# Performance work log

Hardware: AMD Instinct MI355X
Metric: run time of the kernel (lower is better)

Reference implementation:

```python
import jax, jax.numpy as jnp
import numpy as np

M = 16       # learned queries
K = 64       # top-k sparse tokens
HEADS = 4    # attention heads
LN_EPS = 1e-5


def _l2norm(x, eps=1e-12):
    n = jnp.linalg.norm(x, axis=-1, keepdims=True)
    return x / jnp.maximum(n, eps)


def _layernorm(x, w, b):
    mu = x.mean(-1, keepdims=True)
    var = x.var(-1, keepdims=True)
    return (x - mu) * jax.lax.rsqrt(var + LN_EPS) * w + b


def setup_inputs() -> dict:
    key = jax.random.key(0)
    ks = jax.random.split(key, 12)
    B, N, C, T, TD, D = 4, 16384, 1024, 20, 512, 64
    s = lambda k, sh: jax.random.normal(k, sh, jnp.float32) * 0.02
    return {
        "image_features": jax.random.normal(ks[0], (B, N, C), jnp.float32),
        "text_features": jax.random.normal(ks[1], (B, T, TD), jnp.float32),
        "Wd": s(ks[2], (C, D)), "bd": jnp.zeros((D,), jnp.float32),
        "Wu": s(ks[3], (D, C)), "bu": jnp.zeros((C,), jnp.float32),
        "m_queries": jax.random.normal(ks[4], (1, M, D), jnp.float32),
        "Wq": s(ks[5], (D, D)), "bq": jnp.zeros((D,), jnp.float32),
        "Wk": s(ks[6], (D, D)), "bk": jnp.zeros((D,), jnp.float32),
        "Wv": s(ks[7], (D, D)), "bv": jnp.zeros((D,), jnp.float32),
        "Wo": s(ks[8], (D, D)), "bo": jnp.zeros((D,), jnp.float32),
        "ln_w": jnp.ones((D,), jnp.float32), "ln_b": jnp.zeros((D,), jnp.float32),
        "gamma": jnp.float32(0.1),
    }


def reference(image_features, text_features, Wd, bd, Wu, bu, m_queries,
              Wq, bq, Wk, bk, Wv, bv, Wo, bo, ln_w, ln_b, gamma):
    B, N, C = image_features.shape
    D = Wd.shape[1]
    identity = image_features

    # down-project + exact GELU (dropout is identity at eval)
    a = jax.nn.gelu(image_features @ Wd + bd, approximate=False)  # [B,N,D]

    # tokens_of_interest=None, text_consistency_loss=False:
    # slice text to projected dim, take token 0 as key
    sel = text_features[:, 0, :D]                                  # [B,D]
    scores = jnp.einsum("bnd,bd->bn", _l2norm(a), _l2norm(sel))    # [B,N]

    # top-k mask -> nonzero gives row-sorted indices per batch
    _, idx = jax.lax.top_k(scores, K)                              # [B,K]
    idx = jnp.sort(idx, axis=1)

    sparse = jnp.take_along_axis(a, idx[:, :, None], axis=1)       # [B,K,D]
    queries = jnp.broadcast_to(m_queries, (B, M, D))
    comb = jnp.concatenate([queries, sparse], axis=1)              # [B,M+K,D]

    x = _layernorm(comb, ln_w, ln_b)
    H, Dh = HEADS, D // HEADS
    S = M + K
    q = (x @ Wq + bq).reshape(B, S, H, Dh)
    k = (x @ Wk + bk).reshape(B, S, H, Dh)
    v = (x @ Wv + bv).reshape(B, S, H, Dh)
    att = jnp.einsum("bshd,bthd->bhst", q, k) / jnp.sqrt(jnp.float32(Dh))
    att = jax.nn.softmax(att, axis=-1)
    o = jnp.einsum("bhst,bthd->bshd", att, v).reshape(B, S, D)
    attn_out = o @ Wo + bo

    enh = comb + attn_out
    enh_sparse = enh[:, M:, :]                                     # [B,K,D]

    # scatter enhanced sparse tokens back into full sequence
    brow = jnp.arange(B)[:, None]
    delta_proj = jnp.zeros_like(a).at[brow, idx].set(enh_sparse)   # [B,N,D]
    delta_x = delta_proj @ Wu + bu                                 # [B,N,C]

    return identity + delta_x * gamma
```

## Files before the change

kernel.cpp:

```cpp
#include <hip/hip_runtime.h>
#include <hip/hip_bf16.h>
#include <math.h>

typedef __bf16 bf16x8 __attribute__((ext_vector_type(8)));
typedef unsigned short u16x8 __attribute__((ext_vector_type(8)));
typedef float f32x4 __attribute__((ext_vector_type(4)));

#define CDIM 1024
#define DDIM 64
#define NB   16384
#define NROWS 65536

__device__ __forceinline__ unsigned short f2bf(float x){
  unsigned int u = __float_as_uint(x);
  unsigned int lsb = (u >> 16) & 1u;
  u += 0x7fffu + lsb;
  return (unsigned short)(u >> 16);
}

__device__ __forceinline__ void load_lds16(const float* g, float* l){
  __builtin_amdgcn_global_load_lds(
      (const __attribute__((address_space(1))) void*)g,
      (__attribute__((address_space(3))) void*)l, 16, 0, 0);
}

__global__ __launch_bounds__(256) void dsa_prep(
    const float* __restrict__ Wd, const float* __restrict__ tf,
    const float* __restrict__ bu, const float* __restrict__ gam,
    unsigned short* __restrict__ Wf, float* __restrict__ seln,
    float* __restrict__ gbu){
  int bb = blockIdx.x, tid = threadIdx.x;
  if (bb < 32){
    int g = bb*256 + tid;
    int lane = g & 63, tj = g >> 6;
    int n  = ((tj & 3) << 4) + (lane & 15);
    int k0 = ((tj >> 2) << 5) + ((lane >> 4) << 3);
    u16x8 uv;
    #pragma unroll
    for (int e=0;e<8;e++) uv[e] = f2bf(Wd[(k0+e)*DDIM + n]);
    *(u16x8*)(Wf + (size_t)g*8) = uv;
  } else {
    int w = tid >> 6, lane = tid & 63;
    float x = tf[w*(20*512) + lane];
    float sq = x*x;
    #pragma unroll
    for (int m=1; m<64; m<<=1) sq += __shfl_xor(sq, m);
    seln[w*64 + lane] = x / fmaxf(sqrtf(sq), 1e-12f);
    float g = gam[0];
    f32x4 b4 = *(const f32x4*)(bu + tid*4);
    *(f32x4*)(gbu + tid*4) = g*b4;
  }
}

__global__ __launch_bounds__(256, 4) void dsa_main(
    const float* __restrict__ X, const unsigned short* __restrict__ Wf,
    const float* __restrict__ bd, const float* __restrict__ gbu,
    const float* __restrict__ seln,
    float* __restrict__ out, float* __restrict__ a_out, float* __restrict__ scores)
{
  __shared__ __align__(16) float AsF[8192];
  __shared__ __align__(16) float gbS[1024];
  const int tid  = threadIdx.x;
  const int lane = tid & 63, w = tid >> 6;
  const int lr = lane & 15, lq = lane >> 4;
  const int row0 = blockIdx.x*64 + w*16;
  const int batch = blockIdx.x >> 8;

  { f32x4 t = *(const f32x4*)(gbu + tid*4); *(f32x4*)(gbS + tid*4) = t; }
  __syncthreads();

  const int rsub = lane >> 4;
  const int ch   = lane & 15;
  const float* gbase = X + (size_t)(row0 + rsub)*CDIM;
  float* asw = AsF + w*2048;
  float* op  = out + (size_t)(row0 + lr)*CDIM;
  const bf16x8* wf8 = (const bf16x8*)Wf;

  bf16x8 B[8];
  f32x4 acc[4] = {};

#define DMA(P, SL) { \
    { int gc = ch ^ ((0*4 + rsub)&7); \
      load_lds16(gbase + (size_t)(0*4)*CDIM + (P)*64 + gc*4, asw + (SL)*1024 + 0*256); } \
    { int gc = ch ^ ((1*4 + rsub)&7); \
      load_lds16(gbase + (size_t)(1*4)*CDIM + (P)*64 + gc*4, asw + (SL)*1024 + 1*256); } \
    { int gc = ch ^ ((2*4 + rsub)&7); \
      load_lds16(gbase + (size_t)(2*4)*CDIM + (P)*64 + gc*4, asw + (SL)*1024 + 2*256); } \
    { int gc = ch ^ ((3*4 + rsub)&7); \
      load_lds16(gbase + (size_t)(3*4)*CDIM + (P)*64 + gc*4, asw + (SL)*1024 + 3*256); } }

#define LDB(P) { \
    B[0] = wf8[(((P)*2+0)*4+0)*64 + lane]; \
    B[1] = wf8[(((P)*2+0)*4+1)*64 + lane]; \
    B[2] = wf8[(((P)*2+0)*4+2)*64 + lane]; \
    B[3] = wf8[(((P)*2+0)*4+3)*64 + lane]; \
    B[4] = wf8[(((P)*2+1)*4+0)*64 + lane]; \
    B[5] = wf8[(((P)*2+1)*4+1)*64 + lane]; \
    B[6] = wf8[(((P)*2+1)*4+2)*64 + lane]; \
    B[7] = wf8[(((P)*2+1)*4+3)*64 + lane]; }

#define STEP(P, S, SL) { \
    int c0 = (((S)*8 + lq*2 + 0) ^ (lr & 7)); \
    int c1 = (((S)*8 + lq*2 + 1) ^ (lr & 7)); \
    f32x4 xa = *(const f32x4*)(asw + (SL)*1024 + lr*64 + c0*4); \
    f32x4 xb = *(const f32x4*)(asw + (SL)*1024 + lr*64 + c1*4); \
    f32x4 g0 = *(const f32x4*)(gbS + (P)*64 + (S)*32 + lq*8); \
    f32x4 g1 = *(const f32x4*)(gbS + (P)*64 + (S)*32 + lq*8 + 4); \
    *(f32x4*)(op + (P)*64 + (S)*32 + lq*8)     = xa + g0; \
    *(f32x4*)(op + (P)*64 + (S)*32 + lq*8 + 4) = xb + g1; \
    bf16x8 av; \
    av[0]=(__bf16)xa[0]; av[1]=(__bf16)xa[1]; av[2]=(__bf16)xa[2]; av[3]=(__bf16)xa[3]; \
    av[4]=(__bf16)xb[0]; av[5]=(__bf16)xb[1]; av[6]=(__bf16)xb[2]; av[7]=(__bf16)xb[3]; \
    acc[0] = __builtin_amdgcn_mfma_f32_16x16x32_bf16(av, B[4*(S)+0], acc[0], 0,0,0); \
    acc[1] = __builtin_amdgcn_mfma_f32_16x16x32_bf16(av, B[4*(S)+1], acc[1], 0,0,0); \
    acc[2] = __builtin_amdgcn_mfma_f32_16x16x32_bf16(av, B[4*(S)+2], acc[2], 0,0,0); \
    acc[3] = __builtin_amdgcn_mfma_f32_16x16x32_bf16(av, B[4*(S)+3], acc[3], 0,0,0); }

#define PH(P) { \
    DMA((P)+1, ((P)+1)&1) \
    LDB(P) \
    asm volatile("s_waitcnt vmcnt(12)" ::: "memory"); \
    STEP(P, 0, (P)&1) STEP(P, 1, (P)&1) \
    asm volatile("" ::: "memory"); }

  DMA(0, 0)
  PH(0)  PH(1)  PH(2)  PH(3)  PH(4)  PH(5)  PH(6)  PH(7)
  PH(8)  PH(9)  PH(10) PH(11) PH(12) PH(13) PH(14)
  LDB(15)
  asm volatile("s_waitcnt vmcnt(8)" ::: "memory");
  STEP(15, 0, 1) STEP(15, 1, 1)

#undef DMA
#undef LDB
#undef STEP
#undef PH

  const float* selb = seln + batch*64;
  float ss[4] = {0,0,0,0}, dt[4] = {0,0,0,0};
  float gv[4][4];
  #pragma unroll
  for (int j=0;j<4;j++){
    int col = 16*j + lr;
    float bdc = bd[col];
    float sc  = selb[col];
    #pragma unroll
    for (int r=0;r<4;r++){
      float y = acc[j][r] + bdc;
      float g = 0.5f * y * (1.0f + erff(y * 0.70710678118654752f));
      gv[j][r] = g;
      ss[r] += g*g;
      dt[r] += g*sc;
    }
  }
  #pragma unroll
  for (int r=0;r<4;r++){
    int row = row0 + 4*lq + r;
    #pragma unroll
    for (int j=0;j<4;j++)
      a_out[(size_t)row*DDIM + 16*j + lr] = gv[j][r];
  }
  #pragma unroll
  for (int m=1;m<16;m<<=1){
    #pragma unroll
    for (int r=0;r<4;r++){
      ss[r] += __shfl_xor(ss[r], m);
      dt[r] += __shfl_xor(dt[r], m);
    }
  }
  if (lr == 0){
    #pragma unroll
    for (int r=0;r<4;r++)
      scores[row0 + 4*lq + r] = dt[r] / fmaxf(sqrtf(ss[r]), 1e-12f);
  }
}

__global__ __launch_bounds__(1024) void dsa_topk(const float* __restrict__ scores,
                                                 int* __restrict__ idxo){
  const int b = blockIdx.x, tid = threadIdx.x;
  const float* s = scores + b*NB;
  const int base = tid*16;
  unsigned key[16];
  #pragma unroll
  for (int i=0;i<16;i+=4){
    f32x4 f = *(const f32x4*)(s + base + i);
    #pragma unroll
    for (int c=0;c<4;c++){
      unsigned u = __float_as_uint(f[c]);
      key[i+c] = (u & 0x80000000u) ? ~u : (u | 0x80000000u);
    }
  }

  __shared__ unsigned bins[256];
  __shared__ unsigned sh_pref, sh_R;
  __shared__ int selIdx[64];
  __shared__ int eqIdx[256];
  __shared__ unsigned selCnt, eqCnt;

  unsigned prefix = 0, R = 64;
  for (int pass=0; pass<4; ++pass){
    const int shift = 24 - pass*8;
    if (tid < 256) bins[tid] = 0;
    __syncthreads();
    #pragma unroll
    for (int i=0;i<16;i++){
      unsigned k = key[i];
      bool ok;
      if (pass == 0) ok = true;
      else           ok = ((k >> (shift+8)) == prefix);
      if (ok) atomicAdd(&bins[(k >> shift) & 255u], 1u);
    }
    __syncthreads();
    if (tid < 64){
      unsigned c0 = bins[tid*4+0], c1 = bins[tid*4+1];
      unsigned c2 = bins[tid*4+2], c3 = bins[tid*4+3];
      unsigned gs = c0+c1+c2+c3;
      unsigned suf = gs;
      #pragma unroll
      for (int m=1;m<64;m<<=1){
        unsigned o = __shfl_down(suf, m);
        if (tid + m < 64) suf += o;
      }
      unsigned above = suf - gs;
      if (above < R && R <= suf){
        unsigned a3 = above;
        unsigned a2 = a3 + c3;
        unsigned a1 = a2 + c2;
        unsigned a0 = a1 + c1;
        unsigned bb, ab;
        if      (R <= a3 + c3){ bb = 3; ab = a3; }
        else if (R <= a2 + c2){ bb = 2; ab = a2; }
        else if (R <= a1 + c1){ bb = 1; ab = a1; }
        else                  { bb = 0; ab = a0; }
        sh_pref = (prefix << 8) | (tid*4 + bb);
        sh_R = R - ab;
      }
    }
    __syncthreads();
    prefix = sh_pref; R = sh_R;
    __syncthreads();
  }
  if (tid == 0){ selCnt = 0; eqCnt = 0; }
  __syncthreads();
  #pragma unroll
  for (int i=0;i<16;i++){
    unsigned k = key[i];
    if (k > prefix){
      selIdx[atomicAdd(&selCnt, 1u)] = base + i;
    } else if (k == prefix){
      unsigned p = atomicAdd(&eqCnt, 1u);
      if (p < 256) eqIdx[p] = base + i;
    }
  }
  __syncthreads();
  if (tid == 0){
    unsigned n = eqCnt < 256u ? eqCnt : 256u;
    unsigned have = selCnt;
    for (unsigned r2 = 0; r2 < R; ++r2){
      int best = 0x7fffffff, bi = -1;
      for (unsigned e=0; e<n; e++)
        if (eqIdx[e] < best){ best = eqIdx[e]; bi = (int)e; }
      selIdx[have + r2] = best;
      eqIdx[bi] = 0x7fffffff;
    }
  }
  __syncthreads();
  if (tid < 64){
    int x = selIdx[tid];
    #pragma unroll
    for (int size=2; size<=64; size<<=1){
      #pragma unroll
      for (int stride=size>>1; stride>0; stride>>=1){
        int ox = __shfl_xor(x, stride);
        bool up = ((tid & size) == 0);
        bool takeMin = (((tid & stride) == 0) == up);
        int mn = x < ox ? x : ox, mx = x < ox ? ox : x;
        x = takeMin ? mn : mx;
      }
    }
    idxo[b*64 + tid] = x;
  }
}

__global__ __launch_bounds__(512) void dsa_tail(
    const float* __restrict__ a, const float* __restrict__ mq, const int* __restrict__ idx,
    const float* __restrict__ lnw, const float* __restrict__ lnb,
    const float* __restrict__ Wq, const float* __restrict__ bq,
    const float* __restrict__ Wk, const float* __restrict__ bk,
    const float* __restrict__ Wv, const float* __restrict__ bv,
    const float* __restrict__ Wo, const float* __restrict__ bo,
    float* __restrict__ enh)
{
  __shared__ float xln[80][64];
  __shared__ float qS[80][64];
  __shared__ float vS[80][68];
  __shared__ float kT[64][81];
  __shared__ float oS[80][64];
  __shared__ float WoS[64][64];
  __shared__ float rowbuf[8][84];
  __shared__ int   sidx[64];

  const int b = blockIdx.x, tid = threadIdx.x;
  const int w = tid >> 6, lane = tid & 63;

  if (tid < 64) sidx[tid] = idx[b*64 + tid];
  for (int e = tid; e < 4096; e += 512) WoS[e>>6][e&63] = Wo[e];
  __syncthreads();

  {
    float lw = lnw[lane], lb = lnb[lane];
    float vals[10];
    #pragma unroll
    for (int i=0;i<10;i++){
      int s = w + 8*i;
      vals[i] = (s < 16) ? mq[s*64 + lane]
                         : a[((size_t)b*NB + sidx[s-16])*64 + lane];
    }
    #pragma unroll
    for (int i=0;i<10;i++){
      int s = w + 8*i;
      float val = vals[i];
      float sm = val, sq = val*val;
      #pragma unroll
      for (int m=1;m<64;m<<=1){ sm += __shfl_xor(sm,m); sq += __shfl_xor(sq,m); }
      float mu  = sm * (1.0f/64.0f);
      float var = sq * (1.0f/64.0f) - mu*mu;
      xln[s][lane] = (val - mu) * rsqrtf(var + 1e-5f) * lw + lb;
    }
  }
  __syncthreads();

  #pragma unroll 1
  for (int m = 0; m < 3; ++m){
    const float* Wm = (m==0) ? Wq : (m==1) ? Wk : Wv;
    const float* bm = (m==0) ? bq : (m==1) ? bk : bv;
    float wreg[64];
    #pragma unroll
    for (int c=0;c<64;c++) wreg[c] = Wm[c*64 + lane];
    float bias = bm[lane];
    #pragma unroll 1
    for (int s = w; s < 80; s += 8){
      float accv = bias;
      #pragma unroll
      for (int c4=0;c4<16;c4++){
        f32x4 x4 = *(const f32x4*)&xln[s][c4*4];
        accv += x4[0]*wreg[c4*4+0] + x4[1]*wreg[c4*4+1]
              + x4[2]*wreg[c4*4+2] + x4[3]*wreg[c4*4+3];
      }
      if (m==0)      qS[s][lane]  = accv;
      else if (m==1) kT[lane][s]  = accv;
      else           vS[s][lane]  = accv;
    }
  }
  __syncthreads();

  {
    const int h = w >> 1, h16 = h*16;
    const int i0 = 16 + (w & 1)*32;
    const int jj = lane >> 4, dd = lane & 15;
    #pragma unroll 2
    for (int ii = 0; ii < 32; ++ii){
      int i = i0 + ii;
      float v0 = 0.f, v1 = 0.f;
      #pragma unroll
      for (int d=0; d<16; ++d){
        float qd = qS[i][h16+d];
        v0 = fmaf(qd, kT[h16+d][lane],    v0);
        v1 = fmaf(qd, kT[h16+d][64 + dd], v1);
      }
      v0 *= 0.25f; v1 *= 0.25f;
      float mx = fmaxf(v0, v1);
      #pragma unroll
      for (int m2=1;m2<64;m2<<=1) mx = fmaxf(mx, __shfl_xor(mx,m2));
      float e0 = expf(v0 - mx);
      float e1 = expf(v1 - mx);
      float sm = e0 + ((lane < 16) ? e1 : 0.f);
      #pragma unroll
      for (int m2=1;m2<64;m2<<=1) sm += __shfl_xor(sm,m2);
      float inv = 1.0f / sm;
      rowbuf[w][lane] = e0 * inv;
      if (lane < 16) rowbuf[w][64+dd] = e1 * inv;
      float part = 0.f;
      #pragma unroll
      for (int tt=0; tt<20; ++tt){
        int j = jj*20 + tt;
        part = fmaf(rowbuf[w][j], vS[j][h16+dd], part);
      }
      part += __shfl_xor(part, 16);
      part += __shfl_xor(part, 32);
      if (lane < 16) oS[i][h16+dd] = part;
    }
  }
  __syncthreads();

  for (int e = tid; e < 4096; e += 512){
    int s16 = e >> 6, cc = e & 63;
    float accv = bo[cc];
    #pragma unroll
    for (int d4=0; d4<16; ++d4){
      f32x4 o4 = *(const f32x4*)&oS[16+s16][d4*4];
      accv += o4[0]*WoS[d4*4+0][cc] + o4[1]*WoS[d4*4+1][cc]
            + o4[2]*WoS[d4*4+2][cc] + o4[3]*WoS[d4*4+3][cc];
    }
    float cmb = a[((size_t)b*NB + sidx[s16])*64 + cc];
    enh[(b*64 + s16)*64 + cc] = cmb + accv;
  }
}

__global__ __launch_bounds__(256) void dsa_scatter(
    const float* __restrict__ enh, const float* __restrict__ Wu,
    const float* __restrict__ gam, const int* __restrict__ idx,
    float* __restrict__ out)
{
  int blk = blockIdx.x;
  int b = blk >> 6, j = blk & 63;
  int tid = threadIdx.x;
  __shared__ float er[64];
  if (tid < 64) er[tid] = enh[(b*64+j)*64 + tid];
  __syncthreads();
  int n = idx[b*64 + j];
  float gamma = gam[0];
  int c0 = tid*4;
  float ax=0.f, ay=0.f, az=0.f, aw=0.f;
  #pragma unroll 8
  for (int d=0; d<64; ++d){
    float ev = er[d];
    f32x4 wr = *(const f32x4*)(Wu + d*CDIM + c0);
    ax += ev*wr[0]; ay += ev*wr[1]; az += ev*wr[2]; aw += ev*wr[3];
  }
  float* op = out + ((size_t)b*NB + n)*CDIM + c0;
  f32x4 cu = *(f32x4*)op;
  cu[0] += gamma*ax; cu[1] += gamma*ay; cu[2] += gamma*az; cu[3] += gamma*aw;
  *(f32x4*)op = cu;
}

extern "C" void kernel_launch(void* const* d_in, const int* in_sizes, int n_in,
                              void* d_out, int out_size, void* d_ws, size_t ws_size,
                              hipStream_t stream) {
  const float* X    = (const float*)d_in[0];
  const float* tf   = (const float*)d_in[1];
  const float* Wd   = (const float*)d_in[2];
  const float* bd   = (const float*)d_in[3];
  const float* Wu   = (const float*)d_in[4];
  const float* bu   = (const float*)d_in[5];
  const float* mq   = (const float*)d_in[6];
  const float* Wq   = (const float*)d_in[7];
  const float* bq   = (const float*)d_in[8];
  const float* Wk   = (const float*)d_in[9];
  const float* bk   = (const float*)d_in[10];
  const float* Wv   = (const float*)d_in[11];
  const float* bv   = (const float*)d_in[12];
  const float* Wo   = (const float*)d_in[13];
  const float* bo   = (const float*)d_in[14];
  const float* lnw  = (const float*)d_in[15];
  const float* lnb  = (const float*)d_in[16];
  const float* gam  = (const float*)d_in[17];
  float* out = (float*)d_out;

  float* ws_a               = (float*)d_ws;
  unsigned short* ws_wf     = (unsigned short*)(ws_a + (size_t)NROWS*DDIM);
  float* ws_scores          = (float*)(ws_wf + 64*CDIM);
  float* ws_seln            = ws_scores + NROWS;
  float* ws_gbu             = ws_seln + 256;
  int*   ws_idx             = (int*)(ws_gbu + 1024);
  float* ws_enh             = (float*)(ws_idx + 256);

  dsa_prep   <<<33,   256, 0, stream>>>(Wd, tf, bu, gam, ws_wf, ws_seln, ws_gbu);
  dsa_main   <<<1024, 256, 0, stream>>>(X, ws_wf, bd, ws_gbu, ws_seln,
                                        out, ws_a, ws_scores);
  dsa_topk   <<<4,   1024, 0, stream>>>(ws_scores, ws_idx);
  dsa_tail   <<<4,    512, 0, stream>>>(ws_a, mq, ws_idx, lnw, lnb,
                                        Wq, bq, Wk, bk, Wv, bv, Wo, bo, ws_enh);
  dsa_scatter<<<256,  256, 0, stream>>>(ws_enh, Wu, gam, ws_idx, out);
}
```

Measured before the change: 220.8 us.

## Split identity+bias copy out of GEMM kernel and re-pipeline the Wd loads

The residual write (out = X + gamma*bu) moves out of the fused GEMM/score kernel into a separate streaming copy kernel, so X is now read from HBM twice. The GEMM kernel's software pipeline is also reordered: B fragments for the next phase are prefetched after compute and the vmcnt waits are adjusted. The intent is to make the GEMM loop leaner and let the copy run as a simple bandwidth-bound pass, at the cost of an extra full read of the 256MB input.

```diff
diff --git a/kernel.cpp b/kernel.cpp
--- a/kernel.cpp
+++ b/kernel.cpp
@@ -52,28 +52,22 @@
   }
 }
 
-__global__ __launch_bounds__(256, 4) void dsa_main(
+__global__ __launch_bounds__(256, 4) void dsa_gemm(
     const float* __restrict__ X, const unsigned short* __restrict__ Wf,
-    const float* __restrict__ bd, const float* __restrict__ gbu,
-    const float* __restrict__ seln,
-    float* __restrict__ out, float* __restrict__ a_out, float* __restrict__ scores)
+    const float* __restrict__ bd, const float* __restrict__ seln,
+    float* __restrict__ a_out, float* __restrict__ scores)
 {
   __shared__ __align__(16) float AsF[8192];
-  __shared__ __align__(16) float gbS[1024];
   const int tid  = threadIdx.x;
   const int lane = tid & 63, w = tid >> 6;
   const int lr = lane & 15, lq = lane >> 4;
   const int row0 = blockIdx.x*64 + w*16;
   const int batch = blockIdx.x >> 8;
 
-  { f32x4 t = *(const f32x4*)(gbu + tid*4); *(f32x4*)(gbS + tid*4) = t; }
-  __syncthreads();
-
   const int rsub = lane >> 4;
   const int ch   = lane & 15;
   const float* gbase = X + (size_t)(row0 + rsub)*CDIM;
   float* asw = AsF + w*2048;
-  float* op  = out + (size_t)(row0 + lr)*CDIM;
   const bf16x8* wf8 = (const bf16x8*)Wf;
 
   bf16x8 B[8];
@@ -87,7 +81,8 @@
     { int gc = ch ^ ((2*4 + rsub)&7); \
       load_lds16(gbase + (size_t)(2*4)*CDIM + (P)*64 + gc*4, asw + (SL)*1024 + 2*256); } \
     { int gc = ch ^ ((3*4 + rsub)&7); \
-      load_lds16(gbase + (size_t)(3*4)*CDIM + (P)*64 + gc*4, asw + (SL)*1024 + 3*256); } }
+      load_lds16(gbase + (size_t)(3*4)*CDIM + (P)*64 + gc*4, asw + (SL)*1024 + 3*256); } \
+    asm volatile("" ::: "memory"); }
 
 #define LDB(P) { \
     B[0] = wf8[(((P)*2+0)*4+0)*64 + lane]; \
@@ -99,15 +94,11 @@
     B[6] = wf8[(((P)*2+1)*4+2)*64 + lane]; \
     B[7] = wf8[(((P)*2+1)*4+3)*64 + lane]; }
 
-#define STEP(P, S, SL) { \
+#define STEP(S, SL) { \
     int c0 = (((S)*8 + lq*2 + 0) ^ (lr & 7)); \
     int c1 = (((S)*8 + lq*2 + 1) ^ (lr & 7)); \
     f32x4 xa = *(const f32x4*)(asw + (SL)*1024 + lr*64 + c0*4); \
     f32x4 xb = *(const f32x4*)(asw + (SL)*1024 + lr*64 + c1*4); \
-    f32x4 g0 = *(const f32x4*)(gbS + (P)*64 + (S)*32 + lq*8); \
-    f32x4 g1 = *(const f32x4*)(gbS + (P)*64 + (S)*32 + lq*8 + 4); \
-    *(f32x4*)(op + (P)*64 + (S)*32 + lq*8)     = xa + g0; \
-    *(f32x4*)(op + (P)*64 + (S)*32 + lq*8 + 4) = xb + g1; \
     bf16x8 av; \
     av[0]=(__bf16)xa[0]; av[1]=(__bf16)xa[1]; av[2]=(__bf16)xa[2]; av[3]=(__bf16)xa[3]; \
     av[4]=(__bf16)xb[0]; av[5]=(__bf16)xb[1]; av[6]=(__bf16)xb[2]; av[7]=(__bf16)xb[3]; \
@@ -116,19 +107,24 @@
     acc[2] = __builtin_amdgcn_mfma_f32_16x16x32_bf16(av, B[4*(S)+2], acc[2], 0,0,0); \
     acc[3] = __builtin_amdgcn_mfma_f32_16x16x32_bf16(av, B[4*(S)+3], acc[3], 0,0,0); }
 
-#define PH(P) { \
+#define PH(P, W1) { \
+    asm volatile("s_waitcnt vmcnt(" W1 ")" ::: "memory"); \
     DMA((P)+1, ((P)+1)&1) \
-    LDB(P) \
-    asm volatile("s_waitcnt vmcnt(12)" ::: "memory"); \
-    STEP(P, 0, (P)&1) STEP(P, 1, (P)&1) \
+    asm volatile("s_waitcnt vmcnt(4)" ::: "memory"); \
+    STEP(0, (P)&1) STEP(1, (P)&1) \
+    LDB((P)+1) \
     asm volatile("" ::: "memory"); }
 
   DMA(0, 0)
-  PH(0)  PH(1)  PH(2)  PH(3)  PH(4)  PH(5)  PH(6)  PH(7)
-  PH(8)  PH(9)  PH(10) PH(11) PH(12) PH(13) PH(14)
-  LDB(15)
+  LDB(0)
+  DMA(1, 1)
+  PH(0,"12")
+  PH(1,"8")  PH(2,"8")  PH(3,"8")  PH(4,"8")  PH(5,"8")
+  PH(6,"8")  PH(7,"8")  PH(8,"8")  PH(9,"8")  PH(10,"8")
+  PH(11,"8") PH(12,"8") PH(13,"8") PH(14,"8")
   asm volatile("s_waitcnt vmcnt(8)" ::: "memory");
-  STEP(15, 0, 1) STEP(15, 1, 1)
+  asm volatile("s_waitcnt vmcnt(0)" ::: "memory");
+  STEP(0, 1) STEP(1, 1)
 
 #undef DMA
 #undef LDB
@@ -172,6 +168,20 @@
     for (int r=0;r<4;r++)
       scores[row0 + 4*lq + r] = dt[r] / fmaxf(sqrtf(ss[r]), 1e-12f);
   }
+}
+
+__global__ __launch_bounds__(256) void dsa_copy(
+    const float* __restrict__ X, const float* __restrict__ gbu,
+    float* __restrict__ out)
+{
+  const f32x4* x4 = (const f32x4*)X;
+  f32x4*       o4 = (f32x4*)out;
+  const f32x4  gb = ((const f32x4*)gbu)[threadIdx.x];
+  size_t i = (size_t)blockIdx.x*256 + threadIdx.x;
+  const size_t S = (size_t)2048*256;
+  #pragma unroll 8
+  for (int k = 0; k < 32; ++k, i += S)
+    o4[i] = x4[i] + gb;
 }
 
 __global__ __launch_bounds__(1024) void dsa_topk(const float* __restrict__ scores,
@@ -465,10 +475,10 @@
   float* ws_enh             = (float*)(ws_idx + 256);
 
   dsa_prep   <<<33,   256, 0, stream>>>(Wd, tf, bu, gam, ws_wf, ws_seln, ws_gbu);
-  dsa_main   <<<1024, 256, 0, stream>>>(X, ws_wf, bd, ws_gbu, ws_seln,
-                                        out, ws_a, ws_scores);
+  dsa_gemm   <<<1024, 256, 0, stream>>>(X, ws_wf, bd, ws_seln, ws_a, ws_scores);
   dsa_topk   <<<4,   1024, 0, stream>>>(ws_scores, ws_idx);
   dsa_tail   <<<4,    512, 0, stream>>>(ws_a, mq, ws_idx, lnw, lnb,
                                         Wq, bq, Wk, bk, Wv, bv, Wo, bo, ws_enh);
+  dsa_copy   <<<2048, 256, 0, stream>>>(X, ws_gbu, out);
   dsa_scatter<<<256,  256, 0, stream>>>(ws_enh, Wu, gam, ws_idx, out);
 }
```

Result: slower. 273.5 us (+23.9%).
